# Kernel tuning notes

Measured on AMD Instinct MI355X. Metric: run time of the kernel, lower is better.

The kernel has to match this reference:

```python
import jax, jax.numpy as jnp
import numpy as np

B, S, D, H = 2, 2048, 1024, 16
HD = D // H  # head_dim = 64


def setup_inputs() -> dict:
    key = jax.random.key(0)
    ks = jax.random.split(key, 12)
    sc = 0.02
    return {
        "query": jax.random.normal(ks[0], (B, S, D), jnp.float32),
        "key": jax.random.normal(ks[1], (B, S, D), jnp.float32),
        "value": jax.random.normal(ks[2], (B, S, D), jnp.float32),
        "key_padding_mask": jax.random.randint(ks[3], (B, S), 0, 2).astype(bool),
        "attn_mask": jax.random.randint(ks[4], (B, S), 0, 2).astype(bool),
        "is_casual": 0,
        "Wq": jax.random.normal(ks[5], (D, D), jnp.float32) * sc,
        "bq": jnp.zeros((D,), jnp.float32),
        "Wk": jax.random.normal(ks[6], (D, D), jnp.float32) * sc,
        "bk": jnp.zeros((D,), jnp.float32),
        "Wv": jax.random.normal(ks[7], (D, D), jnp.float32) * sc,
        "bv": jnp.zeros((D,), jnp.float32),
        "Wo": jax.random.normal(ks[8], (D, D), jnp.float32) * sc,
        "bo": jnp.zeros((D,), jnp.float32),
    }


def reference(query, key, value, key_padding_mask, attn_mask, is_casual,
              Wq, bq, Wk, bk, Wv, bv, Wo, bo):
    b, s, _ = query.shape
    # projections (torch Linear: x @ W.T + b)
    Q = query @ Wq.T + bq
    K = key @ Wk.T + bk
    V = value @ Wv.T + bv
    # [B, H, S, HD]
    Q = Q.reshape(b, s, H, HD).transpose(0, 2, 1, 3)
    K = K.reshape(b, s, H, HD).transpose(0, 2, 1, 3)
    V = V.reshape(b, s, H, HD).transpose(0, 2, 1, 3)
    scores = jnp.einsum("bhqd,bhkd->bhqk", Q, K) / jnp.sqrt(jnp.float32(HD))
    neg_inf = jnp.float32(-jnp.inf)
    # both masks broadcast over the key axis: [B,1,1,S]
    scores = jnp.where(key_padding_mask[:, None, None, :], neg_inf, scores)
    scores = jnp.where(attn_mask[:, None, None, :], neg_inf, scores)
    # is_casual only applies in training mode; eval reference: no causal mask, no dropout
    attn = jax.nn.softmax(scores, axis=-1)
    x = jnp.einsum("bhqk,bhkd->bhqd", attn, V)
    x = x.transpose(0, 2, 1, 3).reshape(b, s, D)
    return x @ Wo.T + bo
```

## Files before the change

kernel.cpp:

```cpp
#include <hip/hip_runtime.h>


typedef __attribute__((ext_vector_type(8))) short short8;
typedef __attribute__((ext_vector_type(4))) float f32x4;
typedef __attribute__((ext_vector_type(4))) int int32x4;

#define MFMA16(a, b, c) __builtin_amdgcn_mfma_f32_16x16x32_bf16(a, b, c, 0, 0, 0)

#define GLL16(gp, lp) __builtin_amdgcn_global_load_lds( \
    (const __attribute__((address_space(1))) void*)(gp), \
    (__attribute__((address_space(3))) void*)(lp), 16, 0, 0)

static __device__ __forceinline__ unsigned short f2bf(float x) {
    unsigned int u = __float_as_uint(x);
    u = (u + 0x7fffu + ((u >> 16) & 1u)) >> 16;
    return (unsigned short)u;
}

__global__ __launch_bounds__(256)
void scan_kernel(const int* __restrict__ kpm, const int* __restrict__ am,
                 int* __restrict__ map, int* __restrict__ cnt)
{
    const int b = blockIdx.x, tid = threadIdx.x;
    __shared__ int psum[256];
    __shared__ int total_s;
    int flag[8]; int c = 0;
    const int base = b * 2048 + tid * 8;
#pragma unroll
    for (int e = 0; e < 8; ++e) {
        flag[e] = (kpm[base + e] | am[base + e]) ? 0 : 1;
        c += flag[e];
    }
    psum[tid] = c;
    __syncthreads();
    if (tid == 0) {
        int run = 0;
        for (int i = 0; i < 256; ++i) { int t = psum[i]; psum[i] = run; run += t; }
        total_s = run;
        cnt[b] = run;
    }
    __syncthreads();
    int off = b * 2048 + psum[tid];
    const int s0 = tid * 8;
#pragma unroll
    for (int e = 0; e < 8; ++e)
        if (flag[e]) map[off++] = s0 + e;
    __syncthreads();
    const int total = total_s;
    const int first = (total > 0) ? map[b * 2048] : 0;
    for (int j = total + tid; j < 2048; j += 256)
        map[b * 2048 + j] = first;
}

__global__ __launch_bounds__(256)
void conv_many(const float* __restrict__ s0, unsigned short* __restrict__ d0, int n0,
               const float* __restrict__ s1, unsigned short* __restrict__ d1, int n1,
               const float* __restrict__ s2, unsigned short* __restrict__ d2, int n2,
               const float* __restrict__ s3, unsigned short* __restrict__ d3, int n3,
               const float* __restrict__ s4, unsigned short* __restrict__ d4, int n4,
               const float* __restrict__ s5, unsigned short* __restrict__ d5, int n5)
{
    const int y = blockIdx.y;
    const float* s; unsigned short* d; int n;
    if (y == 0)      { s = s0; d = d0; n = n0; }
    else if (y == 1) { s = s1; d = d1; n = n1; }
    else if (y == 2) { s = s2; d = d2; n = n2; }
    else if (y == 3) { s = s3; d = d3; n = n3; }
    else if (y == 4) { s = s4; d = d4; n = n4; }
    else             { s = s5; d = d5; n = n5; }
    const int i = (blockIdx.x * 256 + threadIdx.x) * 8;
    if (i >= n) return;
    const float4 a = *(const float4*)(s + i);
    const float4 b = *(const float4*)(s + i + 4);
    ushort4 lo, hi;
    lo.x = f2bf(a.x); lo.y = f2bf(a.y); lo.z = f2bf(a.z); lo.w = f2bf(a.w);
    hi.x = f2bf(b.x); hi.y = f2bf(b.y); hi.z = f2bf(b.z); hi.w = f2bf(b.w);
    *(ushort4*)(d + i) = lo;
    *(ushort4*)(d + i + 4) = hi;
}

template<int OUT_MODE, bool GATHER>
static __device__ __forceinline__
void gemm_core(int sub, const unsigned short* __restrict__ A, const unsigned short* __restrict__ Wb,
               const float* __restrict__ bias, float alpha, void* __restrict__ outp,
               unsigned short* sm, const int* __restrict__ map, const int* __restrict__ cnt)
{
    constexpr int N = 1024, K = 1024;
    const int xcd = sub & 7, loc = sub >> 3;
    const int m0 = (xcd * 4 + (loc >> 4)) * 128;
    const int n0 = (loc & 15) * 64;

    const int tid = threadIdx.x, lane = tid & 63, wave = tid >> 6;
    const int lr = lane & 15, quad = lane >> 4;
    const int wm = (wave >> 1) * 64, wn = (wave & 1) * 32;
    const int lr3 = lane >> 3;
    const int qcs = (lane & 7) ^ lr3;

    const int bb = m0 >> 11;
    int arow[4];
    if constexpr (GATHER) {
        const int cntb = cnt[bb];
        int cnt64 = (cntb + 63) & ~63;
        if (cnt64 < 64) cnt64 = 64;
        if ((m0 & 2047) >= cnt64) return;
#pragma unroll
        for (int n = 0; n < 4; n++) {
            const int row = (wave * 4 + n) * 8 + lr3;
            arow[n] = bb * 2048 + map[bb * 2048 + (m0 & 2047) + row];
        }
    } else {
#pragma unroll
        for (int n = 0; n < 4; n++)
            arow[n] = m0 + (wave * 4 + n) * 8 + lr3;
    }

    unsigned short* As = sm;
    unsigned short* Bs = sm + 8192;

    f32x4 acc[4][2];
#pragma unroll
    for (int mt = 0; mt < 4; mt++)
#pragma unroll
        for (int nt = 0; nt < 2; nt++) acc[mt][nt] = (f32x4){0.f, 0.f, 0.f, 0.f};

    for (int it = 0; it < 16; ++it) {
        const int k0 = it * 64;
        __syncthreads();
#pragma unroll
        for (int n = 0; n < 4; n++) {
            const int W = wave * 4 + n;
            GLL16(A + (size_t)arow[n] * K + k0 + qcs * 8, As + W * 512);
        }
#pragma unroll
        for (int n = 0; n < 2; n++) {
            const int W = wave * 2 + n;
            const int row = W * 8 + lr3;
            GLL16(Wb + (size_t)(n0 + row) * K + k0 + qcs * 8, Bs + W * 512);
        }
        __syncthreads();
#pragma unroll
        for (int kc = 0; kc < 2; kc++) {
            short8 af[4], bfr[2];
#pragma unroll
            for (int mt = 0; mt < 4; mt++) {
                const int r = wm + mt * 16 + lr;
                af[mt] = *(const short8*)&As[(r * 8 + ((kc * 4 + quad) ^ (r & 7))) * 8];
            }
#pragma unroll
            for (int nt = 0; nt < 2; nt++) {
                const int r = wn + nt * 16 + lr;
                bfr[nt] = *(const short8*)&Bs[(r * 8 + ((kc * 4 + quad) ^ (r & 7))) * 8];
            }
#pragma unroll
            for (int mt = 0; mt < 4; mt++)
#pragma unroll
                for (int nt = 0; nt < 2; nt++)
                    acc[mt][nt] = MFMA16(af[mt], bfr[nt], acc[mt][nt]);
        }
    }

    if constexpr (OUT_MODE == 2) {
        constexpr int LDT = 136;
        __syncthreads();
        unsigned short* Ts = sm;
#pragma unroll
        for (int mt = 0; mt < 4; mt++)
#pragma unroll
            for (int nt = 0; nt < 2; nt++) {
                const int dd = wn + nt * 16 + lr;
                const int ss = wm + mt * 16 + quad * 4;
                const int j = n0 + dd;
                ushort4 tv;
                tv.x = f2bf(alpha * (acc[mt][nt][0] + bias[j]));
                tv.y = f2bf(alpha * (acc[mt][nt][1] + bias[j]));
                tv.z = f2bf(alpha * (acc[mt][nt][2] + bias[j]));
                tv.w = f2bf(alpha * (acc[mt][nt][3] + bias[j]));
                *(ushort4*)&Ts[dd * LDT + ss] = tv;
            }
        __syncthreads();
        const int b = m0 >> 11, hh = (n0 >> 6) & 15, sbase = m0 & 2047;
        const int row = tid >> 2, c4 = (tid & 3) * 32;
        unsigned short* dst = (unsigned short*)outp
            + (((size_t)(b * 16 + hh) * 64) + row) * 2048 + sbase + c4;
#pragma unroll
        for (int t = 0; t < 4; ++t)
            *(short8*)&dst[t * 8] = *(const short8*)&Ts[row * LDT + c4 + t * 8];
        return;
    }

#pragma unroll
    for (int mt = 0; mt < 4; mt++)
#pragma unroll
        for (int nt = 0; nt < 2; nt++)
#pragma unroll
            for (int r = 0; r < 4; r++) {
                const int i = m0 + wm + mt * 16 + quad * 4 + r;
                const int j = n0 + wn + nt * 16 + lr;
                const float val = alpha * (acc[mt][nt][r] + bias[j]);
                if constexpr (OUT_MODE == 0) {
                    ((float*)outp)[(size_t)i * N + j] = val;
                } else {
                    const int b = i >> 11, s = i & 2047, hh = j >> 6, dd = j & 63;
                    ((unsigned short*)outp)[(((size_t)(b * 16 + hh) * 2048) + s) * 64 + dd] = f2bf(val);
                }
            }
}

__global__ __launch_bounds__(256)
void gemm_qv(const unsigned short* __restrict__ qb, const unsigned short* __restrict__ wqb,
             const float* __restrict__ bq, float alpha_q, void* __restrict__ Qh,
             const unsigned short* __restrict__ vb, const unsigned short* __restrict__ wvb,
             const float* __restrict__ bv, void* __restrict__ Vt,
             const int* __restrict__ map, const int* __restrict__ cnt)
{
    __shared__ unsigned short sm[12288];
    const int id = blockIdx.x, sub = id & 511;
    if (id < 512) gemm_core<1, false>(sub, qb, wqb, bq, alpha_q, Qh, sm, nullptr, nullptr);
    else          gemm_core<2, true >(sub, vb, wvb, bv, 1.0f,   Vt, sm, map, cnt);
}

template<int OUT_MODE, bool GATHER>
__global__ __launch_bounds__(256)
void gemm_one(const unsigned short* __restrict__ A, const unsigned short* __restrict__ Wb,
              const float* __restrict__ bias, float alpha, void* __restrict__ outp,
              const int* __restrict__ map, const int* __restrict__ cnt)
{
    __shared__ unsigned short sm[12288];
    gemm_core<OUT_MODE, GATHER>(blockIdx.x, A, Wb, bias, alpha, outp, sm, map, cnt);
}

__global__ __launch_bounds__(256)
void attn_kernel(const unsigned short* __restrict__ Qh, const unsigned short* __restrict__ Kh,
                 const unsigned short* __restrict__ Vt, const int* __restrict__ kpm,
                 const int* __restrict__ am, unsigned short* __restrict__ ctx)
{
    const int qb = blockIdx.x, bh = blockIdx.y, b = bh >> 4, h = bh & 15;
    const int q0 = qb * 64;
    const int tid = threadIdx.x, lane = tid & 63, wave = tid >> 6;
    const int lr = lane & 15, quad = lane >> 4;

    __shared__ unsigned short Ks[2][64 * 64];
    __shared__ unsigned short Vs[2][64 * 64];
    __shared__ int wred[4];

    {
        int c = 0;
        const int mb = b * 2048 + tid * 8;
#pragma unroll
        for (int e = 0; e < 8; ++e)
            c += (kpm[mb + e] | am[mb + e]) ? 0 : 1;
#pragma unroll
        for (int off = 32; off > 0; off >>= 1)
            c += __shfl_xor(c, off, 64);
        if (lane == 0) wred[wave] = c;
    }
    __syncthreads();
    const int cntb = wred[0] + wred[1] + wred[2] + wred[3];
    const int nits = (cntb > 0) ? ((cntb + 63) >> 6) : 1;

    const unsigned short* Kbh = Kh + (size_t)bh * 2048 * 64;
    const unsigned short* Vbh = Vt + (size_t)bh * 64 * 2048;

    const int lr3 = lane >> 3;
    const int qcs = (lane & 7) ^ lr3;

    auto stage = [&](int buf, int k0) {
#pragma unroll
        for (int n = 0; n < 2; ++n) {
            const int W = wave + n * 4;
            const int r = W * 8 + lr3;
            GLL16(Kbh + (size_t)(k0 + r) * 64 + qcs * 8, &Ks[buf][W * 512]);
            GLL16(Vbh + (size_t)r * 2048 + k0 + qcs * 8, &Vs[buf][W * 512]);
        }
    };

    const unsigned short* Qbase = Qh + ((size_t)bh * 2048 + q0 + wave * 16 + lr) * 64 + quad * 8;
    const short8 qf0 = *(const short8*)Qbase;
    const short8 qf1 = *(const short8*)(Qbase + 32);

    short8 onesA;
#pragma unroll
    for (int j = 0; j < 8; j++) onesA[j] = (short)0x3F80;

    f32x4 o[4];
    f32x4 lacc = (f32x4){0.f, 0.f, 0.f, 0.f};
#pragma unroll
    for (int nt = 0; nt < 4; nt++) o[nt] = (f32x4){0.f, 0.f, 0.f, 0.f};

    const int srcA = (quad & 1) * 32 + lr;
    const int srcB = srcA + 16;

    int koff[2][2][2], voff[2][4];
#pragma unroll
    for (int s32 = 0; s32 < 2; ++s32) {
#pragma unroll
        for (int tt = 0; tt < 2; ++tt) {
            const int kk = (s32 * 2 + tt) * 16 + lr;
            koff[s32][tt][0] = (kk * 8 + (quad ^ (kk & 7))) * 8;
            koff[s32][tt][1] = (kk * 8 + ((quad + 4) ^ (kk & 7))) * 8;
        }
#pragma unroll
        for (int nt = 0; nt < 4; ++nt) {
            const int d = nt * 16 + lr;
            const int qc = s32 * 4 + quad;
            voff[s32][nt] = (d * 8 + (qc ^ (d & 7))) * 8;
        }
    }

    auto tile = [&](const unsigned short* __restrict__ Kb,
                    const unsigned short* __restrict__ Vb, int k0) {
#pragma unroll
        for (int s32 = 0; s32 < 2; ++s32) {
            unsigned int pk[2][2];
#pragma unroll
            for (int tt = 0; tt < 2; ++tt) {
                const short8 kf0 = *(const short8*)&Kb[koff[s32][tt][0]];
                const short8 kf1 = *(const short8*)&Kb[koff[s32][tt][1]];
                f32x4 z;
                if (k0 + 64 <= cntb) {
                    z = (f32x4){0.f, 0.f, 0.f, 0.f};
                } else {
                    const int jb = k0 + (s32 * 2 + tt) * 16 + quad * 4;
#pragma unroll
                    for (int r = 0; r < 4; ++r)
                        z[r] = (jb + r < cntb) ? 0.f : -1e5f;
                }
                z = MFMA16(kf0, qf0, z);
                z = MFMA16(kf1, qf1, z);
                const float p0 = __builtin_amdgcn_exp2f(z[0]);
                const float p1 = __builtin_amdgcn_exp2f(z[1]);
                const float p2 = __builtin_amdgcn_exp2f(z[2]);
                const float p3 = __builtin_amdgcn_exp2f(z[3]);
                pk[tt][0] = ((unsigned)f2bf(p1) << 16) | f2bf(p0);
                pk[tt][1] = ((unsigned)f2bf(p3) << 16) | f2bf(p2);
            }
            const int a0 = __shfl((int)pk[0][0], srcA, 64);
            const int a1 = __shfl((int)pk[0][1], srcA, 64);
            const int a2 = __shfl((int)pk[0][0], srcB, 64);
            const int a3 = __shfl((int)pk[0][1], srcB, 64);
            const int c0 = __shfl((int)pk[1][0], srcA, 64);
            const int c1 = __shfl((int)pk[1][1], srcA, 64);
            const int c2 = __shfl((int)pk[1][0], srcB, 64);
            const int c3 = __shfl((int)pk[1][1], srcB, 64);
            const bool hi = quad >= 2;
            union { int32x4 i; short8 s; } u;
            u.i = (int32x4){hi ? c0 : a0, hi ? c1 : a1, hi ? c2 : a2, hi ? c3 : a3};
            const short8 pb = u.s;

            lacc = MFMA16(onesA, pb, lacc);
#pragma unroll
            for (int nt = 0; nt < 4; ++nt) {
                const short8 vf = *(const short8*)&Vb[voff[s32][nt]];
                o[nt] = MFMA16(vf, pb, o[nt]);
            }
        }
    };

    stage(0, 0);

    for (int it = 0; it < nits; ++it) {
        __syncthreads();
        if (it + 1 < nits) stage((it + 1) & 1, (it + 1) * 64);
        if (it & 1) tile(Ks[1], Vs[1], it * 64);
        else        tile(Ks[0], Vs[0], it * 64);
    }

    const float linv = 1.f / lacc[0];
    const int srow = q0 + wave * 16 + lr;
#pragma unroll
    for (int nt = 0; nt < 4; ++nt) {
        ushort4 pk4;
        pk4.x = f2bf(o[nt][0] * linv);
        pk4.y = f2bf(o[nt][1] * linv);
        pk4.z = f2bf(o[nt][2] * linv);
        pk4.w = f2bf(o[nt][3] * linv);
        *(ushort4*)&ctx[((size_t)(b * 2048 + srow)) * 1024 + h * 64 + nt * 16 + quad * 4] = pk4;
    }
}

extern "C" void kernel_launch(void* const* d_in, const int* in_sizes, int n_in,
                              void* d_out, int out_size, void* d_ws, size_t ws_size,
                              hipStream_t stream)
{
    const float* query = (const float*)d_in[0];
    const float* key_  = (const float*)d_in[1];
    const float* value = (const float*)d_in[2];
    const int* kpm     = (const int*)d_in[3];
    const int* am      = (const int*)d_in[4];
    const float* Wq = (const float*)d_in[6];
    const float* bq = (const float*)d_in[7];
    const float* Wk = (const float*)d_in[8];
    const float* bk = (const float*)d_in[9];
    const float* Wv = (const float*)d_in[10];
    const float* bv = (const float*)d_in[11];
    const float* Wo = (const float*)d_in[12];
    const float* bo = (const float*)d_in[13];

    unsigned short* ws16 = (unsigned short*)d_ws;
    unsigned short* Qh  = ws16;
    unsigned short* kbn = ws16 + (1u << 22);
    unsigned short* wob = ws16 + (1u << 22);
    unsigned short* Vt  = ws16 + (2u << 22);
    unsigned short* ctx = ws16 + 3 * (1u << 22);
    unsigned short* wqb = ctx;
    unsigned short* wvb = ctx + (1u << 20);
    unsigned short* wkb = ctx + (2u << 20);
    int* map = (int*)(ctx + (3u << 20));
    int* cnt = map + 4096;

    unsigned short* ob  = (unsigned short*)d_out;
    unsigned short* qb  = ob;
    unsigned short* vb  = ob + (1u << 22);
    unsigned short* Khd = ob;

    const dim3 blk(256);
    const float alpha_q = 0.125f * 1.4426950408889634f;

    scan_kernel<<<2, blk, 0, stream>>>(kpm, am, map, cnt);
    conv_many<<<dim3(2048, 6), blk, 0, stream>>>(
        query, qb,  1 << 22,
        value, vb,  1 << 22,
        key_,  kbn, 1 << 22,
        Wq,    wqb, 1 << 20,
        Wv,    wvb, 1 << 20,
        Wk,    wkb, 1 << 20);
    gemm_qv<<<1024, blk, 0, stream>>>(qb, wqb, bq, alpha_q, (void*)Qh, vb, wvb, bv, (void*)Vt,
                                      map, cnt);
    gemm_one<1, true><<<512, blk, 0, stream>>>(kbn, wkb, bk, 1.0f, (void*)Khd, map, cnt);
    conv_many<<<dim3(512, 1), blk, 0, stream>>>(
        Wo, wob, 1 << 20,
        nullptr, nullptr, 0, nullptr, nullptr, 0,
        nullptr, nullptr, 0, nullptr, nullptr, 0, nullptr, nullptr, 0);
    attn_kernel<<<dim3(32, 32), blk, 0, stream>>>(Qh, Khd, Vt, kpm, am, ctx);
    gemm_one<0, false><<<512, blk, 0, stream>>>(ctx, wob, bo, 1.0f, d_out, nullptr, nullptr);
}
```

Measured before the change: 211.6 us.

## Double-buffer GEMM LDS tiles and use wave-shuffle prefix scan in mask scan

The GEMM core now keeps two LDS stages and issues the global-to-LDS loads for the next K tile before computing on the current one, so load latency can overlap the MFMA work. This costs one barrier per iteration and doubles the LDS allocation to 48KB per block, which may lower occupancy. Separately, the mask scan kernel replaces its serial single-thread prefix sum with a wavefront shuffle scan plus a four-entry cross-wave combine, removing a serialized loop and one barrier.

```diff
diff --git a/kernel.cpp b/kernel.cpp
--- a/kernel.cpp
+++ b/kernel.cpp
@@ -22,8 +22,8 @@
                  int* __restrict__ map, int* __restrict__ cnt)
 {
     const int b = blockIdx.x, tid = threadIdx.x;
-    __shared__ int psum[256];
-    __shared__ int total_s;
+    const int lane = tid & 63, wave = tid >> 6;
+    __shared__ int wtot[4];
     int flag[8]; int c = 0;
     const int base = b * 2048 + tid * 8;
 #pragma unroll
@@ -31,22 +31,25 @@
         flag[e] = (kpm[base + e] | am[base + e]) ? 0 : 1;
         c += flag[e];
     }
-    psum[tid] = c;
+    int pre = c;
+#pragma unroll
+    for (int off = 1; off < 64; off <<= 1) {
+        const int t = __shfl_up(pre, off, 64);
+        if (lane >= off) pre += t;
+    }
+    if (lane == 63) wtot[wave] = pre;
     __syncthreads();
-    if (tid == 0) {
-        int run = 0;
-        for (int i = 0; i < 256; ++i) { int t = psum[i]; psum[i] = run; run += t; }
-        total_s = run;
-        cnt[b] = run;
-    }
-    __syncthreads();
-    int off = b * 2048 + psum[tid];
+    int woff = 0;
+#pragma unroll
+    for (int w = 0; w < 4; ++w) if (w < wave) woff += wtot[w];
+    const int total = wtot[0] + wtot[1] + wtot[2] + wtot[3];
+    if (tid == 0) cnt[b] = total;
+    int off = b * 2048 + woff + (pre - c);
     const int s0 = tid * 8;
 #pragma unroll
     for (int e = 0; e < 8; ++e)
         if (flag[e]) map[off++] = s0 + e;
     __syncthreads();
-    const int total = total_s;
     const int first = (total > 0) ? map[b * 2048] : 0;
     for (int j = total + tid; j < 2048; j += 256)
         map[b * 2048 + j] = first;
@@ -114,42 +117,48 @@
             arow[n] = m0 + (wave * 4 + n) * 8 + lr3;
     }
 
-    unsigned short* As = sm;
-    unsigned short* Bs = sm + 8192;
-
     f32x4 acc[4][2];
 #pragma unroll
     for (int mt = 0; mt < 4; mt++)
 #pragma unroll
         for (int nt = 0; nt < 2; nt++) acc[mt][nt] = (f32x4){0.f, 0.f, 0.f, 0.f};
 
-    for (int it = 0; it < 16; ++it) {
-        const int k0 = it * 64;
-        __syncthreads();
+    auto stg = [&](int t) {
+        unsigned short* Asb = sm + (t & 1) * 12288;
+        unsigned short* Bsb = Asb + 8192;
+        const int k0 = t * 64;
 #pragma unroll
         for (int n = 0; n < 4; n++) {
             const int W = wave * 4 + n;
-            GLL16(A + (size_t)arow[n] * K + k0 + qcs * 8, As + W * 512);
+            GLL16(A + (size_t)arow[n] * K + k0 + qcs * 8, Asb + W * 512);
         }
 #pragma unroll
         for (int n = 0; n < 2; n++) {
             const int W = wave * 2 + n;
             const int row = W * 8 + lr3;
-            GLL16(Wb + (size_t)(n0 + row) * K + k0 + qcs * 8, Bs + W * 512);
-        }
+            GLL16(Wb + (size_t)(n0 + row) * K + k0 + qcs * 8, Bsb + W * 512);
+        }
+    };
+
+    stg(0);
+
+    for (int it = 0; it < 16; ++it) {
         __syncthreads();
+        if (it + 1 < 16) stg(it + 1);
+        const unsigned short* Asc = sm + (it & 1) * 12288;
+        const unsigned short* Bsc = Asc + 8192;
 #pragma unroll
         for (int kc = 0; kc < 2; kc++) {
             short8 af[4], bfr[2];
 #pragma unroll
             for (int mt = 0; mt < 4; mt++) {
                 const int r = wm + mt * 16 + lr;
-                af[mt] = *(const short8*)&As[(r * 8 + ((kc * 4 + quad) ^ (r & 7))) * 8];
+                af[mt] = *(const short8*)&Asc[(r * 8 + ((kc * 4 + quad) ^ (r & 7))) * 8];
             }
 #pragma unroll
             for (int nt = 0; nt < 2; nt++) {
                 const int r = wn + nt * 16 + lr;
-                bfr[nt] = *(const short8*)&Bs[(r * 8 + ((kc * 4 + quad) ^ (r & 7))) * 8];
+                bfr[nt] = *(const short8*)&Bsc[(r * 8 + ((kc * 4 + quad) ^ (r & 7))) * 8];
             }
 #pragma unroll
             for (int mt = 0; mt < 4; mt++)
@@ -213,7 +222,7 @@
              const float* __restrict__ bv, void* __restrict__ Vt,
              const int* __restrict__ map, const int* __restrict__ cnt)
 {
-    __shared__ unsigned short sm[12288];
+    __shared__ unsigned short sm[24576];
     const int id = blockIdx.x, sub = id & 511;
     if (id < 512) gemm_core<1, false>(sub, qb, wqb, bq, alpha_q, Qh, sm, nullptr, nullptr);
     else          gemm_core<2, true >(sub, vb, wvb, bv, 1.0f,   Vt, sm, map, cnt);
@@ -225,7 +234,7 @@
               const float* __restrict__ bias, float alpha, void* __restrict__ outp,
               const int* __restrict__ map, const int* __restrict__ cnt)
 {
-    __shared__ unsigned short sm[12288];
+    __shared__ unsigned short sm[24576];
     gemm_core<OUT_MODE, GATHER>(blockIdx.x, A, Wb, bias, alpha, outp, sm, map, cnt);
 }
 
```

Result: faster. 207.1 us (-2.1%).
